# Kernel optimization log

Hardware: AMD Instinct MI355X
Metric: run time of the kernel (lower is better)

The kernel has to match this reference:

```python
import jax, jax.numpy as jnp
import numpy as np
from jax import lax

RADIUS = 2

def make_kernels(radius):
    # Faithfully reproduces the torch __init__, INCLUDING the bug where
    # NE is computed from the already-normalized NW and SE from SW.
    r = radius
    k = 2 * r + 1
    w = np.ones((k, k), dtype=np.float32)
    L = w.copy(); L[:, r + 1:] = 0
    R = w.copy(); R[:, :r] = 0
    U = w.copy(); U[r + 1:, :] = 0
    D = w.copy(); D[:r, :] = 0
    NW, NE, SW, SE = U.copy(), U.copy(), D.copy(), D.copy()
    half = (r + 1) * k
    L = L / half; R = R / half; U = U / half; D = D / half
    NW[:, r + 1:] = 0
    NE[:, :r] = 0
    SW[:, r + 1:] = 0
    SE[:, :r] = 0
    NW = NW / (r + 1) ** 2
    NE = NW / (r + 1) ** 2  # bug in original: uses new NW
    SW = SW / (r + 1) ** 2
    SE = SW / (r + 1) ** 2  # bug in original: uses new SW
    # order matches d channels 0..7 in forward: L,R,U,D,NW,NE,SW,SE
    return jnp.asarray(np.stack([L, R, U, D, NW, NE, SW, SE])[:, None])  # [8,1,k,k]

def setup_inputs() -> dict:
    key = jax.random.key(0)
    x = jax.random.uniform(key, (8, 3, 768, 768), dtype=jnp.float32)
    return {"x": x, "kernels": make_kernels(RADIUS), "iteration": 3}

def reference(x, kernels, iteration):
    B, C, H, W = x.shape
    k = kernels.shape[-1]
    r = (k - 1) // 2
    # fuse the per-channel loop: treat each (image, channel) as its own sample
    xc = x.reshape(B * C, 1, H, W)

    def step(xc, _):
        # all 8 directional box filters in one conv: [BC,8,H,W]
        conv = lax.conv_general_dilated(
            xc, kernels, window_strides=(1, 1), padding=[(r, r), (r, r)],
            dimension_numbers=("NCHW", "OIHW", "NCHW"))
        d = conv - xc                                   # [BC,8,H,W]
        idx = jnp.argmin(jnp.abs(d), axis=1, keepdims=True)
        dm = jnp.take_along_axis(d, idx, axis=1)        # [BC,1,H,W]
        return xc + dm, None

    xc, _ = lax.scan(step, xc, None, length=iteration)
    return xc.reshape(B, C, H, W)
```

## Files before the change

kernel.cpp:

```cpp
#include <hip/hip_runtime.h>
#include <math.h>


typedef float f4v __attribute__((ext_vector_type(4)));
typedef float f2v __attribute__((ext_vector_type(2), aligned(8)));

template<int PW, bool FULL>
__device__ __forceinline__ void swf_row(const float* __restrict__ rp,
        float* Rv, float* Dv, float* SWv, float* SEv,
        float* Uv, float* NWv, float* NEv, float* ctr) {
    const float w15 = 1.0f / 15.0f;
    const float w9  = 1.0f / 9.0f;
    const float w81 = (1.0f / 9.0f) / 9.0f;

    #pragma unroll
    for (int r = 0; r < 5; r++) {
        const float* p = rp + r * PW;
        f4v lo = *(const f4v*)p;
        f4v hi = *(const f4v*)(p + 4);
        float w[8] = {lo.x, lo.y, lo.z, lo.w, hi.x, hi.y, hi.z, hi.w};

        #pragma unroll
        for (int q = 0; q < 6; q++) {
            float a = (r == 0) ? (w15 * w[q]) : fmaf(w15, w[q], Rv[q]);
            a = fmaf(w15, w[q + 1], a);
            a = fmaf(w15, w[q + 2], a);
            Rv[q] = a;
        }

        #pragma unroll
        for (int j = 0; j < 4; j++) {
            if (FULL && r < 3) {
                float u = (r == 0) ? (w15 * w[j]) : fmaf(w15, w[j], Uv[j]);
                u = fmaf(w15, w[j + 1], u);
                u = fmaf(w15, w[j + 2], u);
                u = fmaf(w15, w[j + 3], u);
                u = fmaf(w15, w[j + 4], u);
                Uv[j] = u;
                float nw = (r == 0) ? (w9 * w[j]) : fmaf(w9, w[j], NWv[j]);
                nw = fmaf(w9, w[j + 1], nw);
                nw = fmaf(w9, w[j + 2], nw);
                NWv[j] = nw;
                float ne = (r == 0) ? (w81 * w[j]) : fmaf(w81, w[j], NEv[j]);
                ne = fmaf(w81, w[j + 1], ne);
                ne = fmaf(w81, w[j + 2], ne);
                NEv[j] = ne;
            }
            if (r >= 2) {
                float d = (r == 2) ? (w15 * w[j]) : fmaf(w15, w[j], Dv[j]);
                d = fmaf(w15, w[j + 1], d);
                d = fmaf(w15, w[j + 2], d);
                d = fmaf(w15, w[j + 3], d);
                d = fmaf(w15, w[j + 4], d);
                Dv[j] = d;
                float sw = (r == 2) ? (w9 * w[j]) : fmaf(w9, w[j], SWv[j]);
                sw = fmaf(w9, w[j + 1], sw);
                sw = fmaf(w9, w[j + 2], sw);
                SWv[j] = sw;
                float se = (r == 2) ? (w81 * w[j]) : fmaf(w81, w[j], SEv[j]);
                se = fmaf(w81, w[j + 1], se);
                se = fmaf(w81, w[j + 2], se);
                SEv[j] = se;
                if (r == 2) ctr[j] = w[j + 2];
            }
        }
    }
}

template<int W2, bool LAST>
__device__ __forceinline__ void emit_store(const float* Rv,
        const float* Ua, const float* NWa, const float* NEa,
        const float* Dn, const float* SWn, const float* SEn, const float* ctr,
        float* __restrict__ Y, float* __restrict__ outp,
        int y, int x0, int gy0, int gx0, bool interior) {
    f4v R;
    #pragma unroll
    for (int j = 0; j < 4; j++) {
        const float c  = ctr[j];
        const float e0 = Rv[j]     - c;
        const float e1 = Rv[j + 2] - c;
        const float e2 = Ua[j]     - c;
        const float e3 = Dn[j]     - c;
        const float e4 = NWa[j]    - c;
        const float e5 = NEa[j]    - c;
        const float e6 = SWn[j]    - c;
        const float e7 = SEn[j]    - c;
        float m01 = (fabsf(e1) < fabsf(e0)) ? e1 : e0;
        float m23 = (fabsf(e3) < fabsf(e2)) ? e3 : e2;
        float m45 = (fabsf(e5) < fabsf(e4)) ? e5 : e4;
        float m67 = (fabsf(e7) < fabsf(e6)) ? e7 : e6;
        float mA  = (fabsf(m23) < fabsf(m01)) ? m23 : m01;
        float mB  = (fabsf(m67) < fabsf(m45)) ? m67 : m45;
        float bd  = (fabsf(mB)  < fabsf(mA))  ? mB  : mA;
        const float res = c + bd;
        if (j == 0) R.x = res; else if (j == 1) R.y = res;
        else if (j == 2) R.z = res; else R.w = res;
    }
    if (LAST) {
        *(f4v*)(outp + y * 768 + x0) = R;
    } else if (interior) {
        *(f4v*)(Y + y * W2 + x0) = R;
    } else {
        const bool rowin = ((unsigned)(gy0 + y) < 768u);
        R.x = (rowin && (unsigned)(gx0 + x0 + 0) < 768u) ? R.x : 0.0f;
        R.y = (rowin && (unsigned)(gx0 + x0 + 1) < 768u) ? R.y : 0.0f;
        R.z = (rowin && (unsigned)(gx0 + x0 + 2) < 768u) ? R.z : 0.0f;
        R.w = (rowin && (unsigned)(gx0 + x0 + 3) < 768u) ? R.w : 0.0f;
        *(f4v*)(Y + y * W2 + x0) = R;
    }
}

template<int H2, int W2, bool LAST>
__device__ __forceinline__ void stepv(const float* __restrict__ X,
                                      float* __restrict__ Y,
                                      float* __restrict__ outp,
                                      int gy0, int gx0, int tid) {
    constexpr int PW     = W2 + 4;
    constexpr int STRIPS = W2 / 4;
    constexpr int BA     = 256 / (2 * STRIPS);
    constexpr int BH     = (((H2 + BA - 1) / BA) + 1) & ~1;
    static_assert(BA * BH >= H2, "bands must cover the tile");

    const bool interior = (gy0 >= 0) && (gx0 >= 0) &&
                          (gy0 + H2 <= 768) && (gx0 + W2 <= 768);

    const int chain = tid / STRIPS;
    const int strip = tid - chain * STRIPS;
    if (chain < 2 * BA) {
        const int band = chain >> 1;
        const int par  = chain & 1;
        const int x0   = strip * 4;
        int y = band * BH + par;
        const int yEnd = (band * BH + BH < H2) ? (band * BH + BH) : H2;
        if (y < yEnd) {
            float Rv[6], Dn[4], SWn[4], SEn[4], Uv[4], NWv[4], NEv[4], ctr[4];
            float pD[4], pSW[4], pSE[4];
            swf_row<PW, true>(X + y * PW + x0, Rv, Dn, SWn, SEn, Uv, NWv, NEv, ctr);
            emit_store<W2, LAST>(Rv, Uv, NWv, NEv, Dn, SWn, SEn, ctr,
                                 Y, outp, y, x0, gy0, gx0, interior);
            #pragma unroll
            for (int j = 0; j < 4; j++) { pD[j] = Dn[j]; pSW[j] = SWn[j]; pSE[j] = SEn[j]; }
            #pragma unroll
            for (int it = 1; it < BH / 2; it++) {
                y += 2;
                if (y < yEnd) {
                    swf_row<PW, false>(X + y * PW + x0, Rv, Dn, SWn, SEn,
                                       Uv, NWv, NEv, ctr);
                    emit_store<W2, LAST>(Rv, pD, pSW, pSE, Dn, SWn, SEn, ctr,
                                         Y, outp, y, x0, gy0, gx0, interior);
                    #pragma unroll
                    for (int j = 0; j < 4; j++) { pD[j] = Dn[j]; pSW[j] = SWn[j]; pSE[j] = SEn[j]; }
                }
            }
        }
    }
    __syncthreads();
}

__global__ __launch_bounds__(256, 6) void swf_fused(const float* __restrict__ in,
                                                    float* __restrict__ out) {
    __shared__ __align__(16) float A[44 * 76];
    __shared__ __align__(16) float B[40 * 72];

    const int tid = threadIdx.x;
    const int tx0 = blockIdx.x * 64;
    const int ty0 = blockIdx.y * 32;
    const long long base = (long long)blockIdx.z * (768 * 768);
    const float* inp = in + base;

    for (int i = tid; i < 44 * 38; i += 256) {
        const int ly  = i / 38;
        const int lx2 = i - ly * 38;
        const int gy  = ty0 + ly - 6;
        const int gx  = tx0 + lx2 * 2 - 6;
        f2v v = {0.0f, 0.0f};
        if ((unsigned)gy < 768u) {
            const float* g = inp + gy * 768 + gx;
            if ((unsigned)gx < 767u) {
                v = *(const f2v*)g;
            } else {
                if ((unsigned)gx < 768u)       v.x = g[0];
                if ((unsigned)(gx + 1) < 768u) v.y = g[1];
            }
        }
        *(f2v*)(A + ly * 76 + lx2 * 2) = v;
    }
    __syncthreads();

    stepv<40, 72, false>(A, B, nullptr, ty0 - 4, tx0 - 4, tid);
    stepv<36, 68, false>(B, A, nullptr, ty0 - 2, tx0 - 2, tid);
    stepv<32, 64, true >(A, nullptr,
                         out + base + (long long)ty0 * 768 + tx0, ty0, tx0, tid);
}

extern "C" void kernel_launch(void* const* d_in, const int* in_sizes, int n_in,
                              void* d_out, int out_size, void* d_ws, size_t ws_size,
                              hipStream_t stream) {
    const float* x = (const float*)d_in[0];
    float* out = (float*)d_out;

    dim3 grid(768 / 64, 768 / 32, 24);
    dim3 block(256);
    swf_fused<<<grid, block, 0, stream>>>(x, out);
}
```

Baseline: 187.2 us.

## Rebalance per-thread row assignment with explicit piece tables in each stencil step

Replaces the uniform band/chain split, which left some threads idle and others with long sequential row chains, with hardcoded per-stage tables. These give every one of the 256 threads a short run of 2 or 3 rows with stride 2. The aim is to even out the work so the slowest thread before each barrier finishes sooner. The cost is some redundant first-row work, since more chains now start fresh with a full vertical accumulation. The tables are also specific to the 40/36/32 tile heights.

```diff
diff --git a/kernel.cpp b/kernel.cpp
--- a/kernel.cpp
+++ b/kernel.cpp
@@ -117,42 +117,44 @@
                                       int gy0, int gx0, int tid) {
     constexpr int PW     = W2 + 4;
     constexpr int STRIPS = W2 / 4;
-    constexpr int BA     = 256 / (2 * STRIPS);
-    constexpr int BH     = (((H2 + BA - 1) / BA) + 1) & ~1;
-    static_assert(BA * BH >= H2, "bands must cover the tile");
+    static_assert(H2 == 40 || H2 == 36 || H2 == 32, "piece tables");
 
     const bool interior = (gy0 >= 0) && (gx0 >= 0) &&
                           (gy0 + H2 <= 768) && (gx0 + W2 <= 768);
 
-    const int chain = tid / STRIPS;
-    const int strip = tid - chain * STRIPS;
-    if (chain < 2 * BA) {
-        const int band = chain >> 1;
-        const int par  = chain & 1;
-        const int x0   = strip * 4;
-        int y = band * BH + par;
-        const int yEnd = (band * BH + BH < H2) ? (band * BH + BH) : H2;
-        if (y < yEnd) {
-            float Rv[6], Dn[4], SWn[4], SEn[4], Uv[4], NWv[4], NEv[4], ctr[4];
-            float pD[4], pSW[4], pSE[4];
-            swf_row<PW, true>(X + y * PW + x0, Rv, Dn, SWn, SEn, Uv, NWv, NEv, ctr);
-            emit_store<W2, LAST>(Rv, Uv, NWv, NEv, Dn, SWn, SEn, ctr,
-                                 Y, outp, y, x0, gy0, gx0, interior);
-            #pragma unroll
-            for (int j = 0; j < 4; j++) { pD[j] = Dn[j]; pSW[j] = SWn[j]; pSE[j] = SEn[j]; }
-            #pragma unroll
-            for (int it = 1; it < BH / 2; it++) {
-                y += 2;
-                if (y < yEnd) {
-                    swf_row<PW, false>(X + y * PW + x0, Rv, Dn, SWn, SEn,
-                                       Uv, NWv, NEv, ctr);
-                    emit_store<W2, LAST>(Rv, pD, pSW, pSE, Dn, SWn, SEn, ctr,
-                                         Y, outp, y, x0, gy0, gx0, interior);
-                    #pragma unroll
-                    for (int j = 0; j < 4; j++) { pD[j] = Dn[j]; pSW[j] = SWn[j]; pSE[j] = SEn[j]; }
-                }
-            }
-        }
+    int run, start, len;
+    if constexpr (H2 == 40) {
+        if (tid < 16)      { run = tid & 3;              start = 2 * (tid >> 2);        len = 2; }
+        else if (tid < 48) { run = 4 + ((tid - 16) & 31); start = 0;                    len = 2; }
+        else if (tid < 64) { int u = tid - 48; run = u & 3;        start = 8 + 3 * (u >> 2); len = 3; }
+        else               { int u = tid - 64; run = 4 + (u & 31); start = 2 + 3 * (u >> 5); len = 3; }
+    } else if constexpr (H2 == 36) {
+        if (tid < 108)      { run = tid % 18;                      start = 2 * (tid / 18);     len = 2; }
+        else if (tid < 156) { int u = tid - 108; run = 18 + (u & 15); start = 2 * (u >> 4);    len = 2; }
+        else if (tid < 192) { int u = tid - 156; run = u % 18;        start = 12 + 3 * (u / 18); len = 3; }
+        else                { int u = tid - 192; run = 18 + (u & 15); start = 6 + 3 * (u >> 4);  len = 3; }
+    } else {
+        run = tid & 31; start = 2 * (tid >> 5); len = 2;
+    }
+
+    const int par   = (run >= STRIPS) ? 1 : 0;
+    const int strip = run - par * STRIPS;
+    const int x0    = strip * 4;
+    const int y     = par + 2 * start;
+
+    const float* rp = X + y * PW + x0;
+    float Rv[6], D0[4], S0[4], E0[4], U0[4], N0[4], M0[4], ctr[4];
+    swf_row<PW, true >(rp, Rv, D0, S0, E0, U0, N0, M0, ctr);
+    emit_store<W2, LAST>(Rv, U0, N0, M0, D0, S0, E0, ctr,
+                         Y, outp, y, x0, gy0, gx0, interior);
+    float D1[4], S1[4], E1[4];
+    swf_row<PW, false>(rp + 2 * PW, Rv, D1, S1, E1, U0, N0, M0, ctr);
+    emit_store<W2, LAST>(Rv, D0, S0, E0, D1, S1, E1, ctr,
+                         Y, outp, y + 2, x0, gy0, gx0, interior);
+    if (len == 3) {
+        swf_row<PW, false>(rp + 4 * PW, Rv, D0, S0, E0, U0, N0, M0, ctr);
+        emit_store<W2, LAST>(Rv, D1, S1, E1, D0, S0, E0, ctr,
+                             Y, outp, y + 4, x0, gy0, gx0, interior);
     }
     __syncthreads();
 }
```

After: 184.8 us. About the same (-1.2%).
